# Kernel tuning notes

Measured on AMD Instinct MI355X. Metric: run time of the kernel, lower is better.

## Reference

```python
import jax, jax.numpy as jnp
import numpy as np

B, T, V, E, U = 64, 128, 20000, 512, 1024


def _gru_dir(x_tbe, W, Uw, bi, bh):
    """Keras GRU (reset_after=True, gate order z,r,h). x_tbe: [T,B,E]."""
    # Precompute all input projections in one big GEMM: [T,B,3U]
    xg = jnp.einsum('tbe,eg->tbg', x_tbe, W) + bi

    def step(h, xg_t):
        hg = h @ Uw + bh                       # [B,3U]
        xz, xr, xh = jnp.split(xg_t, 3, axis=-1)
        hz, hr, hh = jnp.split(hg, 3, axis=-1)
        z = jax.nn.sigmoid(xz + hz)            # update gate
        r = jax.nn.sigmoid(xr + hr)            # reset gate
        hcand = jnp.tanh(xh + r * hh)          # reset_after=True form
        h_new = z * h + (1.0 - z) * hcand
        return h_new, h_new

    h0 = jnp.zeros((x_tbe.shape[1], Uw.shape[0]), x_tbe.dtype)
    hT, outs = jax.lax.scan(step, h0, xg)      # outs: [T,B,U]
    return outs, hT


def setup_inputs() -> dict:
    key = jax.random.key(0)
    ks = jax.random.split(key, 8)
    s_in = 1.0 / np.sqrt(E)
    s_rec = 1.0 / np.sqrt(U)
    return {
        'tokens': jax.random.randint(ks[0], (B, T), 0, V),
        'emb': jax.random.normal(ks[1], (V, E), jnp.float32) * 0.05,
        'Wf': jax.random.normal(ks[2], (E, 3 * U), jnp.float32) * s_in,
        'Uf': jax.random.normal(ks[3], (U, 3 * U), jnp.float32) * s_rec,
        'bif': jnp.zeros((3 * U,), jnp.float32),
        'bhf': jnp.zeros((3 * U,), jnp.float32),
        'Wb': jax.random.normal(ks[4], (E, 3 * U), jnp.float32) * s_in,
        'Ub': jax.random.normal(ks[5], (U, 3 * U), jnp.float32) * s_rec,
        'bib': jnp.zeros((3 * U,), jnp.float32),
        'bhb': jnp.zeros((3 * U,), jnp.float32),
    }


def reference(tokens, emb, Wf, Uf, bif, bhf, Wb, Ub, bib, bhb):
    tokens = tokens[:, ::-1]                    # tf.reverse(inputs, [-1])
    x = emb[tokens]                             # embedding lookup -> [B,T,E]
    x_t = jnp.swapaxes(x, 0, 1)                 # [T,B,E]
    out_f, h_f = _gru_dir(x_t, Wf, Uf, bif, bhf)
    out_b, h_b = _gru_dir(x_t[::-1], Wb, Ub, bib, bhb)
    out_b = out_b[::-1]                         # re-align backward outputs
    outputs = jnp.swapaxes(out_f + out_b, 0, 1)  # merge_mode='sum' -> [B,T,U]
    hidden = jnp.concatenate([h_f, h_b], axis=1)  # [B,2U]
    return outputs, hidden
```

## Files before the change

### kernel.cpp

```cpp
#include <hip/hip_runtime.h>
#include <hip/hip_bf16.h>

typedef float f32;
typedef __hip_bfloat16 bf16;
typedef unsigned int u32;
typedef unsigned short u16;

#define T_LEN 128
#define B_SZ  64
#define E_DIM 512
#define U_DIM 1024
#define G3    3072
#define BTU   (B_SZ * T_LEN * U_DIM)

typedef __attribute__((ext_vector_type(8))) __bf16 bf16x8;
typedef __attribute__((ext_vector_type(8))) u16  us8;
typedef __attribute__((ext_vector_type(4))) f32  f32x4;

union F8 { us8 u; bf16x8 b; };

#define WS_USW 0u
#define WS_HQ  25165824u
#define WS_XG  26214400u

__device__ __forceinline__ u32 f32_to_bf16_rne(f32 x) {
  u32 b = __float_as_uint(x);
  return (b + 0x7fffu + ((b >> 16) & 1u)) >> 16;
}

__global__ __launch_bounds__(256) void transpose_split(
    const f32* __restrict__ Uf, const f32* __restrict__ Ub, u16* __restrict__ USW)
{
  __shared__ f32 tile[32][33];
  const int d = blockIdx.z;
  const f32* Uw = d ? Ub : Uf;
  const int c0 = blockIdx.x * 32;
  const int k0 = blockIdx.y * 32;
  const int tx = threadIdx.x & 31;
  const int ty = threadIdx.x >> 5;
#pragma unroll
  for (int i = 0; i < 4; i++) {
    int kl = ty + i * 8;
    tile[kl][tx] = Uw[(size_t)(k0 + kl) * G3 + c0 + tx];
  }
  __syncthreads();
#pragma unroll
  for (int i = 0; i < 4; i++) {
    int cl = ty + i * 8;
    int c  = c0 + cl;
    f32 val = tile[tx][cl];
    int g = c >> 10, u = c & 1023;
    int blk = d * 128 + (u >> 3);
    int r   = g * 8 + (u & 7);
    u32 hib = f32_to_bf16_rne(val);
    f32 rem = val - __uint_as_float(hib << 16);
    u32 lob = f32_to_bf16_rne(rem);
    int k = k0 + tx;
    int slot = (k >> 3) ^ (r & 7);
    size_t base = ((size_t)blk * 2) * (24 * 1024);
    size_t off  = (size_t)r * 1024 + slot * 8 + (k & 7);
    USW[base + off] = (u16)hib;
    USW[base + (size_t)24 * 1024 + off] = (u16)lob;
  }
}

__global__ __launch_bounds__(256) void xg_gemm(
    const int* __restrict__ tokens, const f32* __restrict__ emb,
    const f32* __restrict__ Wf, const f32* __restrict__ bif,
    const f32* __restrict__ Wb, const f32* __restrict__ bib,
    bf16* __restrict__ XG)
{
  __shared__ f32 As[8][128];
  __shared__ f32 Bs[8][128];
  __shared__ int tok_s[128];

  const int tid = threadIdx.x;
  const int n0 = blockIdx.x * 128;
  const int m0 = blockIdx.y * 128;
  const int dir = (m0 >= T_LEN * B_SZ) ? 1 : 0;
  const f32* W  = dir ? Wb : Wf;
  const f32* bi = dir ? bib : bif;

  if (tid < 128) {
    int mm = m0 + tid - dir * (T_LEN * B_SZ);
    int s = mm >> 6, b = mm & 63;
    int t_orig = dir ? s : (T_LEN - 1 - s);
    tok_s[tid] = tokens[b * T_LEN + t_orig];
  }
  __syncthreads();

  const int lr = tid >> 1;
  const int lh = (tid & 1) * 4;
  const int bk = tid >> 5;
  const int bn = (tid & 31) * 4;
  const f32* arow = emb + (size_t)tok_s[lr] * E_DIM + lh;
  const f32* brow = W + (size_t)bk * G3 + n0 + bn;

  const int tm = tid >> 4;
  const int tn = tid & 15;

  f32 acc[8][8];
#pragma unroll
  for (int i = 0; i < 8; i++)
#pragma unroll
    for (int j = 0; j < 8; j++) acc[i][j] = 0.f;

  for (int k0 = 0; k0 < E_DIM; k0 += 8) {
    float4 av = *(const float4*)(arow + k0);
    float4 bv = *(const float4*)(brow + (size_t)k0 * G3);
    __syncthreads();
    As[lh + 0][lr] = av.x;
    As[lh + 1][lr] = av.y;
    As[lh + 2][lr] = av.z;
    As[lh + 3][lr] = av.w;
    *(float4*)&Bs[bk][bn] = bv;
    __syncthreads();
#pragma unroll
    for (int kk = 0; kk < 8; kk++) {
      float4 a0 = *(float4*)&As[kk][tm * 4];
      float4 a1 = *(float4*)&As[kk][64 + tm * 4];
      float4 b0 = *(float4*)&Bs[kk][tn * 4];
      float4 b1 = *(float4*)&Bs[kk][64 + tn * 4];
      f32 am[8] = {a0.x,a0.y,a0.z,a0.w,a1.x,a1.y,a1.z,a1.w};
      f32 bb[8] = {b0.x,b0.y,b0.z,b0.w,b1.x,b1.y,b1.z,b1.w};
#pragma unroll
      for (int i = 0; i < 8; i++)
#pragma unroll
        for (int j = 0; j < 8; j++)
          acc[i][j] += am[i] * bb[j];
    }
  }

  f32 biv[8];
#pragma unroll
  for (int j = 0; j < 8; j++) {
    int nloc = tn * 4 + (j & 3) + (j >> 2) * 64;
    biv[j] = bi[n0 + nloc];
  }
#pragma unroll
  for (int i = 0; i < 8; i++) {
    int mloc = tm * 4 + (i & 3) + (i >> 2) * 64;
    int mm = m0 + mloc - dir * (T_LEN * B_SZ);
    int s = mm >> 6, b = mm & 63;
    size_t rowbase = ((size_t)(dir * T_LEN + s) * G3) * B_SZ + b;
#pragma unroll
    for (int j = 0; j < 8; j++) {
      int nloc = tn * 4 + (j & 3) + (j >> 2) * 64;
      XG[rowbase + (size_t)(n0 + nloc) * B_SZ] = __float2bfloat16(acc[i][j] + biv[j]);
    }
  }
}

__global__ __launch_bounds__(512) void gru_step_mfma(
    const u16* __restrict__ USW,
    u32* __restrict__ Hq,
    const u16* __restrict__ XG,
    const f32* __restrict__ bhf, const f32* __restrict__ bhb,
    f32* __restrict__ out, int s)
{
  extern __shared__ u16 Us[];
  const int blk = blockIdx.x;
  const int dir = blk >> 7;
  const int su  = (blk & 127) * 8;
  const int tid = threadIdx.x;
  const int lane = tid & 63;
  const int w  = tid >> 6;
  const int nw = w & 3, kw = w >> 2;

  {
    const us8* src = (const us8*)(USW + (size_t)blk * (2 * 24 * 1024));
    us8* dst = (us8*)Us;
    for (int i = tid; i < (2 * 24 * 1024) / 8; i += 512) dst[i] = src[i];
  }

  const u32* Hin  = Hq + (size_t)((s & 1) * 2 + dir) * (U_DIM * B_SZ);
  u32*       Hout = Hq + (size_t)(((s + 1) & 1) * 2 + dir) * (U_DIM * B_SZ);

  const int bb = nw * 16 + (lane & 15);
  const int ko = (lane >> 4) * 8;
  const int r0 = lane & 15;
  const int r1t = 16 + (lane & 15);
  const int r1 = r1t > 23 ? 23 : r1t;

  const int rb_h0 = (0 * 24 + r0) * 2048;
  const int rb_l0 = (1 * 24 + r0) * 2048;
  const int rb_h1 = (0 * 24 + r1) * 2048;
  const int rb_l1 = (1 * 24 + r1) * 2048;
  const int sw0 = r0 & 7, sw1 = r1 & 7;

  __syncthreads();

  f32x4 acc0 = {0.f, 0.f, 0.f, 0.f};
  f32x4 acc1 = {0.f, 0.f, 0.f, 0.f};

  for (int ks = 0; ks < 16; ks++) {
    const int kb = kw * 512 + ks * 32;
    const int slot = (kb >> 3) + (lane >> 4);
    F8 ah0, al0, ah1, al1;
    ah0.u = *(const us8*)((const char*)Us + rb_h0 + ((slot ^ sw0) << 4));
    al0.u = *(const us8*)((const char*)Us + rb_l0 + ((slot ^ sw0) << 4));
    ah1.u = *(const us8*)((const char*)Us + rb_h1 + ((slot ^ sw1) << 4));
    al1.u = *(const us8*)((const char*)Us + rb_l1 + ((slot ^ sw1) << 4));

    const int kbase = kb + ko;
    u32 wd[8];
#pragma unroll
    for (int e = 0; e < 8; e++) wd[e] = Hin[(size_t)(kbase + e) * B_SZ + bb];
    F8 bh_hi, bh_lo;
#pragma unroll
    for (int e = 0; e < 8; e++) {
      bh_hi.u[e] = (u16)(wd[e] & 0xffffu);
      bh_lo.u[e] = (u16)(wd[e] >> 16);
    }
    acc0 = __builtin_amdgcn_mfma_f32_16x16x32_bf16(ah0.b, bh_hi.b, acc0, 0, 0, 0);
    acc0 = __builtin_amdgcn_mfma_f32_16x16x32_bf16(ah0.b, bh_lo.b, acc0, 0, 0, 0);
    acc0 = __builtin_amdgcn_mfma_f32_16x16x32_bf16(al0.b, bh_hi.b, acc0, 0, 0, 0);
    acc1 = __builtin_amdgcn_mfma_f32_16x16x32_bf16(ah1.b, bh_hi.b, acc1, 0, 0, 0);
    acc1 = __builtin_amdgcn_mfma_f32_16x16x32_bf16(ah1.b, bh_lo.b, acc1, 0, 0, 0);
    acc1 = __builtin_amdgcn_mfma_f32_16x16x32_bf16(al1.b, bh_hi.b, acc1, 0, 0, 0);
  }

  __syncthreads();
  f32* red = (f32*)Us;
  if (kw == 1) {
    f32* p = red + (size_t)(nw * 64 + lane) * 8;
    *(f32x4*)p = acc0;
    *(f32x4*)(p + 4) = acc1;
  }
  __syncthreads();
  if (kw == 0) {
    const f32* p = red + (size_t)(nw * 64 + lane) * 8;
    f32x4 o0 = *(const f32x4*)p;
    f32x4 o1 = *(const f32x4*)(p + 4);
#pragma unroll
    for (int i = 0; i < 4; i++) { acc0[i] += o0[i]; acc1[i] += o1[i]; }

    const f32* bh = dir ? bhb : bhf;
    f32 racc[4];
#pragma unroll
    for (int j = 0; j < 4; j++) racc[j] = __shfl_xor(acc0[j], 32);

    if (lane < 32) {
      const size_t xgb = ((size_t)(dir * T_LEN + s) * G3) * B_SZ + bb;
      const int t = dir ? (T_LEN - 1 - s) : s;
#pragma unroll
      for (int j = 0; j < 4; j++) {
        const int ul = (lane >> 4) * 4 + j;
        const int u  = su + ul;
        f32 hz = acc0[j] + bh[u];
        f32 hr = racc[j] + bh[1024 + u];
        f32 hh = acc1[j] + bh[2048 + u];
        f32 xz = __uint_as_float((u32)XG[xgb + (size_t)u * B_SZ] << 16);
        f32 xr = __uint_as_float((u32)XG[xgb + (size_t)(1024 + u) * B_SZ] << 16);
        f32 xh = __uint_as_float((u32)XG[xgb + (size_t)(2048 + u) * B_SZ] << 16);

        u32 hw = Hin[(size_t)u * B_SZ + bb];
        f32 hold = __uint_as_float(hw << 16) + __uint_as_float(hw & 0xffff0000u);

        f32 z  = 1.f / (1.f + expf(-(xz + hz)));
        f32 r  = 1.f / (1.f + expf(-(xr + hr)));
        f32 hc = tanhf(xh + r * hh);
        f32 hnew = z * hold + (1.f - z) * hc;

        u32 hib = f32_to_bf16_rne(hnew);
        f32 rem = hnew - __uint_as_float(hib << 16);
        u32 lob = f32_to_bf16_rne(rem);
        Hout[(size_t)u * B_SZ + bb] = hib | (lob << 16);

        size_t oidx = ((size_t)bb * T_LEN + t) * U_DIM + u;
        if (s < 64) out[oidx] = hnew;
        else        out[oidx] += hnew;

        if (s == T_LEN - 1)
          out[(size_t)BTU + (size_t)bb * 2048 + dir * 1024 + u] = hnew;
      }
    }
  }
}

extern "C" void kernel_launch(void* const* d_in, const int* in_sizes, int n_in,
                              void* d_out, int out_size, void* d_ws, size_t ws_size,
                              hipStream_t stream) {
  (void)in_sizes; (void)n_in; (void)out_size; (void)ws_size;
  const int* tokens = (const int*)d_in[0];
  const f32* emb = (const f32*)d_in[1];
  const f32* Wf  = (const f32*)d_in[2];
  const f32* Uf  = (const f32*)d_in[3];
  const f32* bif = (const f32*)d_in[4];
  const f32* bhf = (const f32*)d_in[5];
  const f32* Wb  = (const f32*)d_in[6];
  const f32* Ub  = (const f32*)d_in[7];
  const f32* bib = (const f32*)d_in[8];
  const f32* bhb = (const f32*)d_in[9];

  char* ws = (char*)d_ws;
  u16*  USW = (u16*)(ws + WS_USW);
  u32*  Hq  = (u32*)(ws + WS_HQ);
  bf16* XG  = (bf16*)(ws + WS_XG);
  f32*  out = (f32*)d_out;

  hipMemsetAsync(Hq, 0, (size_t)2 * 2 * U_DIM * B_SZ * sizeof(u32), stream);
  transpose_split<<<dim3(96, 32, 2), 256, 0, stream>>>(Uf, Ub, USW);
  xg_gemm<<<dim3(24, 128), 256, 0, stream>>>(tokens, emb, Wf, bif, Wb, bib, XG);

  hipFuncSetAttribute((const void*)gru_step_mfma,
                      hipFuncAttributeMaxDynamicSharedMemorySize, 98304);
  for (int s = 0; s < T_LEN; s++)
    gru_step_mfma<<<256, 512, 98304, stream>>>(USW, Hq, (const u16*)XG, bhf, bhb, out, s);
}
```

Measured before the change: 2.172 ms.

## Replace per-timestep kernel launches with persistent cooperative kernel and grid barrier

```diff
diff --git a/kernel.cpp b/kernel.cpp
--- a/kernel.cpp
+++ b/kernel.cpp
@@ -22,6 +22,9 @@
 #define WS_USW 0u
 #define WS_HQ  25165824u
 #define WS_XG  26214400u
+#define WS_BAR 126877696u
+
+#define LDS_BYTES 106496
 
 __device__ __forceinline__ u32 f32_to_bf16_rne(f32 x) {
   u32 b = __float_as_uint(x);
@@ -151,12 +154,13 @@
   }
 }
 
-__global__ __launch_bounds__(512) void gru_step_mfma(
+__global__ __launch_bounds__(512) void gru_persist(
     const u16* __restrict__ USW,
     u32* __restrict__ Hq,
     const u16* __restrict__ XG,
     const f32* __restrict__ bhf, const f32* __restrict__ bhb,
-    f32* __restrict__ out, int s)
+    f32* __restrict__ out,
+    u32* __restrict__ bar)
 {
   extern __shared__ u16 Us[];
   const int blk = blockIdx.x;
@@ -170,11 +174,8 @@
   {
     const us8* src = (const us8*)(USW + (size_t)blk * (2 * 24 * 1024));
     us8* dst = (us8*)Us;
-    for (int i = tid; i < (2 * 24 * 1024) / 8; i += 512) dst[i] = src[i];
-  }
-
-  const u32* Hin  = Hq + (size_t)((s & 1) * 2 + dir) * (U_DIM * B_SZ);
-  u32*       Hout = Hq + (size_t)(((s + 1) & 1) * 2 + dir) * (U_DIM * B_SZ);
+    for (int i = tid; i < 6144; i += 512) dst[i] = src[i];
+  }
 
   const int bb = nw * 16 + (lane & 15);
   const int ko = (lane >> 4) * 8;
@@ -188,93 +189,112 @@
   const int rb_l1 = (1 * 24 + r1) * 2048;
   const int sw0 = r0 & 7, sw1 = r1 & 7;
 
+  f32* red = (f32*)(Us + 49152);
+  const f32* bh = dir ? bhb : bhf;
+
   __syncthreads();
 
-  f32x4 acc0 = {0.f, 0.f, 0.f, 0.f};
-  f32x4 acc1 = {0.f, 0.f, 0.f, 0.f};
-
-  for (int ks = 0; ks < 16; ks++) {
-    const int kb = kw * 512 + ks * 32;
-    const int slot = (kb >> 3) + (lane >> 4);
-    F8 ah0, al0, ah1, al1;
-    ah0.u = *(const us8*)((const char*)Us + rb_h0 + ((slot ^ sw0) << 4));
-    al0.u = *(const us8*)((const char*)Us + rb_l0 + ((slot ^ sw0) << 4));
-    ah1.u = *(const us8*)((const char*)Us + rb_h1 + ((slot ^ sw1) << 4));
-    al1.u = *(const us8*)((const char*)Us + rb_l1 + ((slot ^ sw1) << 4));
-
-    const int kbase = kb + ko;
-    u32 wd[8];
-#pragma unroll
-    for (int e = 0; e < 8; e++) wd[e] = Hin[(size_t)(kbase + e) * B_SZ + bb];
-    F8 bh_hi, bh_lo;
-#pragma unroll
-    for (int e = 0; e < 8; e++) {
-      bh_hi.u[e] = (u16)(wd[e] & 0xffffu);
-      bh_lo.u[e] = (u16)(wd[e] >> 16);
-    }
-    acc0 = __builtin_amdgcn_mfma_f32_16x16x32_bf16(ah0.b, bh_hi.b, acc0, 0, 0, 0);
-    acc0 = __builtin_amdgcn_mfma_f32_16x16x32_bf16(ah0.b, bh_lo.b, acc0, 0, 0, 0);
-    acc0 = __builtin_amdgcn_mfma_f32_16x16x32_bf16(al0.b, bh_hi.b, acc0, 0, 0, 0);
-    acc1 = __builtin_amdgcn_mfma_f32_16x16x32_bf16(ah1.b, bh_hi.b, acc1, 0, 0, 0);
-    acc1 = __builtin_amdgcn_mfma_f32_16x16x32_bf16(ah1.b, bh_lo.b, acc1, 0, 0, 0);
-    acc1 = __builtin_amdgcn_mfma_f32_16x16x32_bf16(al1.b, bh_hi.b, acc1, 0, 0, 0);
-  }
-
-  __syncthreads();
-  f32* red = (f32*)Us;
-  if (kw == 1) {
-    f32* p = red + (size_t)(nw * 64 + lane) * 8;
-    *(f32x4*)p = acc0;
-    *(f32x4*)(p + 4) = acc1;
-  }
-  __syncthreads();
-  if (kw == 0) {
-    const f32* p = red + (size_t)(nw * 64 + lane) * 8;
-    f32x4 o0 = *(const f32x4*)p;
-    f32x4 o1 = *(const f32x4*)(p + 4);
-#pragma unroll
-    for (int i = 0; i < 4; i++) { acc0[i] += o0[i]; acc1[i] += o1[i]; }
-
-    const f32* bh = dir ? bhb : bhf;
-    f32 racc[4];
-#pragma unroll
-    for (int j = 0; j < 4; j++) racc[j] = __shfl_xor(acc0[j], 32);
-
-    if (lane < 32) {
-      const size_t xgb = ((size_t)(dir * T_LEN + s) * G3) * B_SZ + bb;
-      const int t = dir ? (T_LEN - 1 - s) : s;
-#pragma unroll
-      for (int j = 0; j < 4; j++) {
-        const int ul = (lane >> 4) * 4 + j;
-        const int u  = su + ul;
-        f32 hz = acc0[j] + bh[u];
-        f32 hr = racc[j] + bh[1024 + u];
-        f32 hh = acc1[j] + bh[2048 + u];
-        f32 xz = __uint_as_float((u32)XG[xgb + (size_t)u * B_SZ] << 16);
-        f32 xr = __uint_as_float((u32)XG[xgb + (size_t)(1024 + u) * B_SZ] << 16);
-        f32 xh = __uint_as_float((u32)XG[xgb + (size_t)(2048 + u) * B_SZ] << 16);
-
-        u32 hw = Hin[(size_t)u * B_SZ + bb];
-        f32 hold = __uint_as_float(hw << 16) + __uint_as_float(hw & 0xffff0000u);
-
-        f32 z  = 1.f / (1.f + expf(-(xz + hz)));
-        f32 r  = 1.f / (1.f + expf(-(xr + hr)));
-        f32 hc = tanhf(xh + r * hh);
-        f32 hnew = z * hold + (1.f - z) * hc;
-
-        u32 hib = f32_to_bf16_rne(hnew);
-        f32 rem = hnew - __uint_as_float(hib << 16);
-        u32 lob = f32_to_bf16_rne(rem);
-        Hout[(size_t)u * B_SZ + bb] = hib | (lob << 16);
-
-        size_t oidx = ((size_t)bb * T_LEN + t) * U_DIM + u;
-        if (s < 64) out[oidx] = hnew;
-        else        out[oidx] += hnew;
-
-        if (s == T_LEN - 1)
-          out[(size_t)BTU + (size_t)bb * 2048 + dir * 1024 + u] = hnew;
+  for (int s = 0; s < T_LEN; s++) {
+    const u32* Hin  = Hq + (size_t)((s & 1) * 2 + dir) * (U_DIM * B_SZ);
+    u32*       Hout = Hq + (size_t)(((s + 1) & 1) * 2 + dir) * (U_DIM * B_SZ);
+
+    f32x4 acc0 = {0.f, 0.f, 0.f, 0.f};
+    f32x4 acc1 = {0.f, 0.f, 0.f, 0.f};
+
+    if (s) {
+      for (int ks = 0; ks < 16; ks++) {
+        const int kb = kw * 512 + ks * 32;
+        const int slot = (kb >> 3) + (lane >> 4);
+        F8 ah0, al0, ah1, al1;
+        ah0.u = *(const us8*)((const char*)Us + rb_h0 + ((slot ^ sw0) << 4));
+        al0.u = *(const us8*)((const char*)Us + rb_l0 + ((slot ^ sw0) << 4));
+        ah1.u = *(const us8*)((const char*)Us + rb_h1 + ((slot ^ sw1) << 4));
+        al1.u = *(const us8*)((const char*)Us + rb_l1 + ((slot ^ sw1) << 4));
+
+        const int kbase = kb + ko;
+        u32 wd[8];
+#pragma unroll
+        for (int e = 0; e < 8; e++) wd[e] = Hin[(size_t)(kbase + e) * B_SZ + bb];
+        F8 bh_hi, bh_lo;
+#pragma unroll
+        for (int e = 0; e < 8; e++) {
+          bh_hi.u[e] = (u16)(wd[e] & 0xffffu);
+          bh_lo.u[e] = (u16)(wd[e] >> 16);
+        }
+        acc0 = __builtin_amdgcn_mfma_f32_16x16x32_bf16(ah0.b, bh_hi.b, acc0, 0, 0, 0);
+        acc0 = __builtin_amdgcn_mfma_f32_16x16x32_bf16(ah0.b, bh_lo.b, acc0, 0, 0, 0);
+        acc0 = __builtin_amdgcn_mfma_f32_16x16x32_bf16(al0.b, bh_hi.b, acc0, 0, 0, 0);
+        acc1 = __builtin_amdgcn_mfma_f32_16x16x32_bf16(ah1.b, bh_hi.b, acc1, 0, 0, 0);
+        acc1 = __builtin_amdgcn_mfma_f32_16x16x32_bf16(ah1.b, bh_lo.b, acc1, 0, 0, 0);
+        acc1 = __builtin_amdgcn_mfma_f32_16x16x32_bf16(al1.b, bh_hi.b, acc1, 0, 0, 0);
       }
     }
+
+    __syncthreads();
+    if (kw == 1) {
+      f32* p = red + (size_t)(nw * 64 + lane) * 8;
+      *(f32x4*)p = acc0;
+      *(f32x4*)(p + 4) = acc1;
+    }
+    __syncthreads();
+    if (kw == 0) {
+      const f32* p = red + (size_t)(nw * 64 + lane) * 8;
+      f32x4 o0 = *(const f32x4*)p;
+      f32x4 o1 = *(const f32x4*)(p + 4);
+#pragma unroll
+      for (int i = 0; i < 4; i++) { acc0[i] += o0[i]; acc1[i] += o1[i]; }
+
+      f32 racc[4];
+#pragma unroll
+      for (int j = 0; j < 4; j++) racc[j] = __shfl_xor(acc0[j], 32);
+
+      if (lane < 32) {
+        const size_t xgb = ((size_t)(dir * T_LEN + s) * G3) * B_SZ + bb;
+        const int t = dir ? (T_LEN - 1 - s) : s;
+#pragma unroll
+        for (int j = 0; j < 4; j++) {
+          const int ul = (lane >> 4) * 4 + j;
+          const int u  = su + ul;
+          f32 hz = acc0[j] + bh[u];
+          f32 hr = racc[j] + bh[1024 + u];
+          f32 hh = acc1[j] + bh[2048 + u];
+          f32 xz = __uint_as_float((u32)XG[xgb + (size_t)u * B_SZ] << 16);
+          f32 xr = __uint_as_float((u32)XG[xgb + (size_t)(1024 + u) * B_SZ] << 16);
+          f32 xh = __uint_as_float((u32)XG[xgb + (size_t)(2048 + u) * B_SZ] << 16);
+
+          u32 hw = s ? Hin[(size_t)u * B_SZ + bb] : 0u;
+          f32 hold = __uint_as_float(hw << 16) + __uint_as_float(hw & 0xffff0000u);
+
+          f32 z  = 1.f / (1.f + expf(-(xz + hz)));
+          f32 r  = 1.f / (1.f + expf(-(xr + hr)));
+          f32 hc = tanhf(xh + r * hh);
+          f32 hnew = z * hold + (1.f - z) * hc;
+
+          u32 hib = f32_to_bf16_rne(hnew);
+          f32 rem = hnew - __uint_as_float(hib << 16);
+          u32 lob = f32_to_bf16_rne(rem);
+          Hout[(size_t)u * B_SZ + bb] = hib | (lob << 16);
+
+          size_t oidx = ((size_t)bb * T_LEN + t) * U_DIM + u;
+          if (s < 64) out[oidx] = hnew;
+          else        out[oidx] += hnew;
+
+          if (s == T_LEN - 1)
+            out[(size_t)BTU + (size_t)bb * 2048 + dir * 1024 + u] = hnew;
+        }
+      }
+    }
+
+    __syncthreads();
+    if (tid == 0) {
+      __threadfence();
+      __hip_atomic_fetch_add(bar, 1u, __ATOMIC_RELAXED, __HIP_MEMORY_SCOPE_AGENT);
+      const u32 tgt = 256u * (u32)(s + 1);
+      while (__hip_atomic_load(bar, __ATOMIC_RELAXED, __HIP_MEMORY_SCOPE_AGENT) < tgt)
+        __builtin_amdgcn_s_sleep(2);
+      __threadfence();
+    }
+    __syncthreads();
   }
 }
 
@@ -297,14 +317,24 @@
   u16*  USW = (u16*)(ws + WS_USW);
   u32*  Hq  = (u32*)(ws + WS_HQ);
   bf16* XG  = (bf16*)(ws + WS_XG);
+  u32*  bar = (u32*)(ws + WS_BAR);
   f32*  out = (f32*)d_out;
 
-  hipMemsetAsync(Hq, 0, (size_t)2 * 2 * U_DIM * B_SZ * sizeof(u32), stream);
+  hipMemsetAsync(bar, 0, sizeof(u32), stream);
   transpose_split<<<dim3(96, 32, 2), 256, 0, stream>>>(Uf, Ub, USW);
   xg_gemm<<<dim3(24, 128), 256, 0, stream>>>(tokens, emb, Wf, bif, Wb, bib, XG);
 
-  hipFuncSetAttribute((const void*)gru_step_mfma,
-                      hipFuncAttributeMaxDynamicSharedMemorySize, 98304);
-  for (int s = 0; s < T_LEN; s++)
-    gru_step_mfma<<<256, 512, 98304, stream>>>(USW, Hq, (const u16*)XG, bhf, bhb, out, s);
-}
+  hipFuncSetAttribute((const void*)gru_persist,
+                      hipFuncAttributeMaxDynamicSharedMemorySize, LDS_BYTES);
+  const u16* usw_a = USW;
+  u32*       hq_a  = Hq;
+  const u16* xg_a  = (const u16*)XG;
+  const f32* bhf_a = bhf;
+  const f32* bhb_a = bhb;
+  f32*       out_a = out;
+  u32*       bar_a = bar;
+  void* kargs[] = { (void*)&usw_a, (void*)&hq_a, (void*)&xg_a,
+                    (void*)&bhf_a, (void*)&bhb_a, (void*)&out_a, (void*)&bar_a };
+  hipLaunchCooperativeKernel((const void*)gru_persist, dim3(256), dim3(512),
+                             kargs, LDS_BYTES, stream);
+}
```

Result: slower. 4.654 ms (+114.3%).

## Restructure GRU step with batch-major hidden/XG layouts and 4-way K split

Applied to the files above, without the earlier changes.

```diff
diff --git a/kernel.cpp b/kernel.cpp
--- a/kernel.cpp
+++ b/kernel.cpp
@@ -15,6 +15,7 @@
 
 typedef __attribute__((ext_vector_type(8))) __bf16 bf16x8;
 typedef __attribute__((ext_vector_type(8))) u16  us8;
+typedef __attribute__((ext_vector_type(4))) u16  us4;
 typedef __attribute__((ext_vector_type(4))) f32  f32x4;
 
 union F8 { us8 u; bf16x8 b; };
@@ -22,6 +23,8 @@
 #define WS_USW 0u
 #define WS_HQ  25165824u
 #define WS_XG  26214400u
+
+#define LDS_BYTES (98304 + 24576)
 
 __device__ __forceinline__ u32 f32_to_bf16_rne(f32 x) {
   u32 b = __float_as_uint(x);
@@ -142,18 +145,18 @@
     int mloc = tm * 4 + (i & 3) + (i >> 2) * 64;
     int mm = m0 + mloc - dir * (T_LEN * B_SZ);
     int s = mm >> 6, b = mm & 63;
-    size_t rowbase = ((size_t)(dir * T_LEN + s) * G3) * B_SZ + b;
+    size_t rowbase = ((size_t)(dir * T_LEN + s) * B_SZ + b) * G3;
 #pragma unroll
     for (int j = 0; j < 8; j++) {
       int nloc = tn * 4 + (j & 3) + (j >> 2) * 64;
-      XG[rowbase + (size_t)(n0 + nloc) * B_SZ] = __float2bfloat16(acc[i][j] + biv[j]);
+      XG[rowbase + n0 + nloc] = __float2bfloat16(acc[i][j] + biv[j]);
     }
   }
 }
 
-__global__ __launch_bounds__(512) void gru_step_mfma(
+__global__ __launch_bounds__(1024, 4) void gru_step3(
     const u16* __restrict__ USW,
-    u32* __restrict__ Hq,
+    u16* __restrict__ Hq2,
     const u16* __restrict__ XG,
     const f32* __restrict__ bhf, const f32* __restrict__ bhb,
     f32* __restrict__ out, int s)
@@ -170,14 +173,13 @@
   {
     const us8* src = (const us8*)(USW + (size_t)blk * (2 * 24 * 1024));
     us8* dst = (us8*)Us;
-    for (int i = tid; i < (2 * 24 * 1024) / 8; i += 512) dst[i] = src[i];
-  }
-
-  const u32* Hin  = Hq + (size_t)((s & 1) * 2 + dir) * (U_DIM * B_SZ);
-  u32*       Hout = Hq + (size_t)(((s + 1) & 1) * 2 + dir) * (U_DIM * B_SZ);
+#pragma unroll
+    for (int i = 0; i < 6; i++) dst[tid + i * 1024] = src[tid + i * 1024];
+  }
 
   const int bb = nw * 16 + (lane & 15);
   const int ko = (lane >> 4) * 8;
+  const int kq = kw * 256;
   const int r0 = lane & 15;
   const int r1t = 16 + (lane & 15);
   const int r1 = r1t > 23 ? 23 : r1t;
@@ -188,74 +190,104 @@
   const int rb_l1 = (1 * 24 + r1) * 2048;
   const int sw0 = r0 & 7, sw1 = r1 & 7;
 
+  const int bufr = s & 1, bufw = bufr ^ 1;
+  const u16* HrHi = Hq2 + (size_t)(((bufr * 2 + 0) * 2 + dir) * 64 + bb) * 1024;
+  const u16* HrLo = Hq2 + (size_t)(((bufr * 2 + 1) * 2 + dir) * 64 + bb) * 1024;
+
+  F8 h_hi0, h_lo0, h_hi1, h_lo1, h_hi2, h_lo2, h_hi3, h_lo3;
+  if (s) {
+    const u16* p = HrHi + kq + ko;
+    const u16* q = HrLo + kq + ko;
+    h_hi0.u = *(const us8*)(p);        h_lo0.u = *(const us8*)(q);
+    h_hi1.u = *(const us8*)(p + 32);   h_lo1.u = *(const us8*)(q + 32);
+    h_hi2.u = *(const us8*)(p + 64);   h_lo2.u = *(const us8*)(q + 64);
+    h_hi3.u = *(const us8*)(p + 96);   h_lo3.u = *(const us8*)(q + 96);
+  }
+
   __syncthreads();
 
   f32x4 acc0 = {0.f, 0.f, 0.f, 0.f};
   f32x4 acc1 = {0.f, 0.f, 0.f, 0.f};
 
-  for (int ks = 0; ks < 16; ks++) {
-    const int kb = kw * 512 + ks * 32;
-    const int slot = (kb >> 3) + (lane >> 4);
-    F8 ah0, al0, ah1, al1;
-    ah0.u = *(const us8*)((const char*)Us + rb_h0 + ((slot ^ sw0) << 4));
-    al0.u = *(const us8*)((const char*)Us + rb_l0 + ((slot ^ sw0) << 4));
-    ah1.u = *(const us8*)((const char*)Us + rb_h1 + ((slot ^ sw1) << 4));
-    al1.u = *(const us8*)((const char*)Us + rb_l1 + ((slot ^ sw1) << 4));
-
-    const int kbase = kb + ko;
-    u32 wd[8];
-#pragma unroll
-    for (int e = 0; e < 8; e++) wd[e] = Hin[(size_t)(kbase + e) * B_SZ + bb];
-    F8 bh_hi, bh_lo;
-#pragma unroll
-    for (int e = 0; e < 8; e++) {
-      bh_hi.u[e] = (u16)(wd[e] & 0xffffu);
-      bh_lo.u[e] = (u16)(wd[e] >> 16);
-    }
-    acc0 = __builtin_amdgcn_mfma_f32_16x16x32_bf16(ah0.b, bh_hi.b, acc0, 0, 0, 0);
-    acc0 = __builtin_amdgcn_mfma_f32_16x16x32_bf16(ah0.b, bh_lo.b, acc0, 0, 0, 0);
-    acc0 = __builtin_amdgcn_mfma_f32_16x16x32_bf16(al0.b, bh_hi.b, acc0, 0, 0, 0);
-    acc1 = __builtin_amdgcn_mfma_f32_16x16x32_bf16(ah1.b, bh_hi.b, acc1, 0, 0, 0);
-    acc1 = __builtin_amdgcn_mfma_f32_16x16x32_bf16(ah1.b, bh_lo.b, acc1, 0, 0, 0);
-    acc1 = __builtin_amdgcn_mfma_f32_16x16x32_bf16(al1.b, bh_hi.b, acc1, 0, 0, 0);
-  }
-
-  __syncthreads();
-  f32* red = (f32*)Us;
-  if (kw == 1) {
-    f32* p = red + (size_t)(nw * 64 + lane) * 8;
+#define DOMFMA(HHI, HLO, KS) { \
+    const int slot = (kq >> 3) + (KS) * 4 + (lane >> 4); \
+    F8 ah0, al0, ah1, al1; \
+    ah0.u = *(const us8*)((const char*)Us + rb_h0 + ((slot ^ sw0) << 4)); \
+    al0.u = *(const us8*)((const char*)Us + rb_l0 + ((slot ^ sw0) << 4)); \
+    ah1.u = *(const us8*)((const char*)Us + rb_h1 + ((slot ^ sw1) << 4)); \
+    al1.u = *(const us8*)((const char*)Us + rb_l1 + ((slot ^ sw1) << 4)); \
+    acc0 = __builtin_amdgcn_mfma_f32_16x16x32_bf16(ah0.b, HHI.b, acc0, 0, 0, 0); \
+    acc0 = __builtin_amdgcn_mfma_f32_16x16x32_bf16(ah0.b, HLO.b, acc0, 0, 0, 0); \
+    acc0 = __builtin_amdgcn_mfma_f32_16x16x32_bf16(al0.b, HHI.b, acc0, 0, 0, 0); \
+    acc1 = __builtin_amdgcn_mfma_f32_16x16x32_bf16(ah1.b, HHI.b, acc1, 0, 0, 0); \
+    acc1 = __builtin_amdgcn_mfma_f32_16x16x32_bf16(ah1.b, HLO.b, acc1, 0, 0, 0); \
+    acc1 = __builtin_amdgcn_mfma_f32_16x16x32_bf16(al1.b, HHI.b, acc1, 0, 0, 0); \
+  }
+#define LDH(HHI, HLO, KS) { \
+    HHI.u = *(const us8*)(HrHi + kq + ko + (KS) * 32); \
+    HLO.u = *(const us8*)(HrLo + kq + ko + (KS) * 32); \
+  }
+
+  if (s) {
+    DOMFMA(h_hi0, h_lo0, 0) LDH(h_hi0, h_lo0, 4)
+    DOMFMA(h_hi1, h_lo1, 1) LDH(h_hi1, h_lo1, 5)
+    DOMFMA(h_hi2, h_lo2, 2) LDH(h_hi2, h_lo2, 6)
+    DOMFMA(h_hi3, h_lo3, 3) LDH(h_hi3, h_lo3, 7)
+    DOMFMA(h_hi0, h_lo0, 4)
+    DOMFMA(h_hi1, h_lo1, 5)
+    DOMFMA(h_hi2, h_lo2, 6)
+    DOMFMA(h_hi3, h_lo3, 7)
+  }
+#undef DOMFMA
+#undef LDH
+
+  __syncthreads();
+  f32* red = (f32*)(Us + 49152);
+  if (kw) {
+    f32* p = red + (size_t)(((kw - 1) * 4 + nw) * 64 + lane) * 8;
     *(f32x4*)p = acc0;
     *(f32x4*)(p + 4) = acc1;
   }
   __syncthreads();
   if (kw == 0) {
-    const f32* p = red + (size_t)(nw * 64 + lane) * 8;
-    f32x4 o0 = *(const f32x4*)p;
-    f32x4 o1 = *(const f32x4*)(p + 4);
-#pragma unroll
-    for (int i = 0; i < 4; i++) { acc0[i] += o0[i]; acc1[i] += o1[i]; }
-
-    const f32* bh = dir ? bhb : bhf;
+#pragma unroll
+    for (int g = 0; g < 3; g++) {
+      const f32* p = red + (size_t)((g * 4 + nw) * 64 + lane) * 8;
+      f32x4 o0 = *(const f32x4*)p;
+      f32x4 o1 = *(const f32x4*)(p + 4);
+#pragma unroll
+      for (int i = 0; i < 4; i++) { acc0[i] += o0[i]; acc1[i] += o1[i]; }
+    }
+
     f32 racc[4];
 #pragma unroll
     for (int j = 0; j < 4; j++) racc[j] = __shfl_xor(acc0[j], 32);
 
     if (lane < 32) {
-      const size_t xgb = ((size_t)(dir * T_LEN + s) * G3) * B_SZ + bb;
-      const int t = dir ? (T_LEN - 1 - s) : s;
+      const int ul0 = (lane >> 4) * 4;
+      const int u0 = su + ul0;
+      const u16* xgp = XG + ((size_t)(dir * T_LEN + s) * B_SZ + bb) * G3;
+      us4 gz = *(const us4*)(xgp + u0);
+      us4 gr = *(const us4*)(xgp + 1024 + u0);
+      us4 gh = *(const us4*)(xgp + 2048 + u0);
+      us4 ohi = {0, 0, 0, 0}, olo = {0, 0, 0, 0};
+      if (s) {
+        ohi = *(const us4*)(HrHi + u0);
+        olo = *(const us4*)(HrLo + u0);
+      }
+      const f32* bh = dir ? bhb : bhf;
+      f32x4 hnv;
+      us4 whi, wlo;
 #pragma unroll
       for (int j = 0; j < 4; j++) {
-        const int ul = (lane >> 4) * 4 + j;
-        const int u  = su + ul;
+        const int u = u0 + j;
         f32 hz = acc0[j] + bh[u];
         f32 hr = racc[j] + bh[1024 + u];
         f32 hh = acc1[j] + bh[2048 + u];
-        f32 xz = __uint_as_float((u32)XG[xgb + (size_t)u * B_SZ] << 16);
-        f32 xr = __uint_as_float((u32)XG[xgb + (size_t)(1024 + u) * B_SZ] << 16);
-        f32 xh = __uint_as_float((u32)XG[xgb + (size_t)(2048 + u) * B_SZ] << 16);
-
-        u32 hw = Hin[(size_t)u * B_SZ + bb];
-        f32 hold = __uint_as_float(hw << 16) + __uint_as_float(hw & 0xffff0000u);
+        f32 xz = __uint_as_float((u32)gz[j] << 16);
+        f32 xr = __uint_as_float((u32)gr[j] << 16);
+        f32 xh = __uint_as_float((u32)gh[j] << 16);
+        f32 hold = __uint_as_float((u32)ohi[j] << 16) + __uint_as_float((u32)olo[j] << 16);
 
         f32 z  = 1.f / (1.f + expf(-(xz + hz)));
         f32 r  = 1.f / (1.f + expf(-(xr + hr)));
@@ -265,15 +297,27 @@
         u32 hib = f32_to_bf16_rne(hnew);
         f32 rem = hnew - __uint_as_float(hib << 16);
         u32 lob = f32_to_bf16_rne(rem);
-        Hout[(size_t)u * B_SZ + bb] = hib | (lob << 16);
-
-        size_t oidx = ((size_t)bb * T_LEN + t) * U_DIM + u;
-        if (s < 64) out[oidx] = hnew;
-        else        out[oidx] += hnew;
-
-        if (s == T_LEN - 1)
-          out[(size_t)BTU + (size_t)bb * 2048 + dir * 1024 + u] = hnew;
+        hnv[j] = hnew;
+        whi[j] = (u16)hib;
+        wlo[j] = (u16)lob;
       }
+      u16* HwHi = Hq2 + (size_t)(((bufw * 2 + 0) * 2 + dir) * 64 + bb) * 1024;
+      u16* HwLo = Hq2 + (size_t)(((bufw * 2 + 1) * 2 + dir) * 64 + bb) * 1024;
+      *(us4*)(HwHi + u0) = whi;
+      *(us4*)(HwLo + u0) = wlo;
+
+      const int t = dir ? (T_LEN - 1 - s) : s;
+      f32* op = out + ((size_t)bb * T_LEN + t) * U_DIM + u0;
+      if (s < 64) {
+        *(f32x4*)op = hnv;
+      } else {
+        f32x4 prev = *(const f32x4*)op;
+#pragma unroll
+        for (int j = 0; j < 4; j++) prev[j] += hnv[j];
+        *(f32x4*)op = prev;
+      }
+      if (s == T_LEN - 1)
+        *(f32x4*)(out + (size_t)BTU + (size_t)bb * 2048 + dir * 1024 + u0) = hnv;
     }
   }
 }
@@ -295,16 +339,15 @@
 
   char* ws = (char*)d_ws;
   u16*  USW = (u16*)(ws + WS_USW);
-  u32*  Hq  = (u32*)(ws + WS_HQ);
+  u16*  Hq2 = (u16*)(ws + WS_HQ);
   bf16* XG  = (bf16*)(ws + WS_XG);
   f32*  out = (f32*)d_out;
 
-  hipMemsetAsync(Hq, 0, (size_t)2 * 2 * U_DIM * B_SZ * sizeof(u32), stream);
   transpose_split<<<dim3(96, 32, 2), 256, 0, stream>>>(Uf, Ub, USW);
   xg_gemm<<<dim3(24, 128), 256, 0, stream>>>(tokens, emb, Wf, bif, Wb, bib, XG);
 
-  hipFuncSetAttribute((const void*)gru_step_mfma,
-                      hipFuncAttributeMaxDynamicSharedMemorySize, 98304);
+  hipFuncSetAttribute((const void*)gru_step3,
+                      hipFuncAttributeMaxDynamicSharedMemorySize, LDS_BYTES);
   for (int s = 0; s < T_LEN; s++)
-    gru_step_mfma<<<256, 512, 98304, stream>>>(USW, Hq, (const u16*)XG, bhf, bhb, out, s);
-}
+    gru_step3<<<256, 1024, LDS_BYTES, stream>>>(USW, Hq2, (const u16*)XG, bhf, bhb, out, s);
+}
```

Result: slower. 2.583 ms (+18.9%).
